# Kernel optimization log

Hardware: AMD Instinct MI355X
Metric: run time of the kernel (lower is better)

Reference implementation:

```python
import jax, jax.numpy as jnp
import numpy as np

N, M = 30000, 32
VX, VY, VZ = 0.2, 0.2, 4.0
XOFF, YOFF, ZOFF = 0.1, -39.9, -1.0  # vx/2+pc_range[0], vy/2+pc_range[1], vz/2+pc_range[2]
EPS = 1e-3
H = 3  # num_heads, head_dim = 3 // 3 = 1


def setup_inputs() -> dict:
    key = jax.random.key(0)
    ks = jax.random.split(key, 13)
    features = jax.random.normal(ks[0], (N, M, 4), jnp.float32)
    num_points = jax.random.randint(ks[1], (N,), 1, M + 1, dtype=jnp.int32)
    coors = jax.random.randint(ks[2], (N, 4), 0, 352, dtype=jnp.int32)
    # PFN layer params (Linear 10->64 no bias, BN1d affine)
    pfn_w = jax.random.normal(ks[3], (10, 64), jnp.float32) * 0.1
    bn_gamma = jnp.ones((64,), jnp.float32)
    bn_beta = jnp.zeros((64,), jnp.float32)
    # PillarAttention: MHA on 3-dim coords, 3 heads of dim 1
    wq = jax.random.normal(ks[4], (3, 3), jnp.float32) * 0.5
    wk = jax.random.normal(ks[5], (3, 3), jnp.float32) * 0.5
    wv = jax.random.normal(ks[6], (3, 3), jnp.float32) * 0.5
    wo = jax.random.normal(ks[7], (3, 3), jnp.float32) * 0.5
    bq = jax.random.normal(ks[8], (3,), jnp.float32) * 0.02
    bk = jax.random.normal(ks[9], (3,), jnp.float32) * 0.02
    bv = jax.random.normal(ks[10], (3,), jnp.float32) * 0.02
    bo = jax.random.normal(ks[11], (3,), jnp.float32) * 0.02
    return dict(features=features, num_points=num_points, coors=coors,
                pfn_w=pfn_w, bn_gamma=bn_gamma, bn_beta=bn_beta,
                wq=wq, wk=wk, wv=wv, wo=wo, bq=bq, bk=bk, bv=bv, bo=bo)


def _pillar_attention(xyz, wq, wk, wv, wo, bq, bk, bv, bo):
    # xyz: (N, M, 3); 3 heads of dim 1 -> per-head score is an outer product
    q = xyz @ wq + bq  # (N, M, 3)
    k = xyz @ wk + bk
    v = xyz @ wv + bv
    # head_dim = 1 => scale = 1/sqrt(1) = 1
    scores = jnp.einsum('nih,njh->nhij', q, k)          # (N, H, M, M)
    attn = jax.nn.softmax(scores, axis=-1)
    out = jnp.einsum('nhij,njh->nih', attn, v)          # (N, M, 3)
    return out @ wo + bo


def reference(features, num_points, coors, pfn_w, bn_gamma, bn_beta,
              wq, wk, wv, wo, bq, bk, bv, bo):
    dtype = features.dtype
    xyz = features[:, :, :3]  # original coords (attn & cluster use these, pre in-place write)

    # PillarAttention on raw xyz, then max over feature dim
    feat_attn = _pillar_attention(xyz, wq, wk, wv, wo, bq, bk, bv, bo)  # (N, M, 3)
    max_attn = jnp.max(feat_attn, axis=-1, keepdims=True)              # (N, M, 1)

    npts = num_points.astype(dtype)[:, None, None]                      # (N,1,1)
    # cluster center offsets (uses original xyz)
    points_mean = jnp.sum(xyz, axis=1, keepdims=True) / npts
    f_cluster = xyz - points_mean                                       # (N, M, 3)

    # voxel center offsets; coors = [batch, z, y, x]
    cf = coors.astype(dtype)
    cx = cf[:, 3] * VX + XOFF
    cy = cf[:, 2] * VY + YOFF
    cz = cf[:, 1] * VZ + ZOFF
    f_center = jnp.stack([xyz[:, :, 0] - cx[:, None],
                          xyz[:, :, 1] - cy[:, None],
                          xyz[:, :, 2] - cz[:, None]], axis=-1)          # (N, M, 3)

    # legacy=True in-place bug: features[:, :, :3] becomes f_center before concat
    feats = jnp.concatenate([f_center, features[:, :, 3:], f_cluster, f_center], axis=-1)  # (N, M, 10)

    # mask out padded points
    mask = (jnp.arange(M)[None, :] < num_points[:, None]).astype(dtype)[:, :, None]
    feats = feats * mask

    # PFNLayer (last_vfe=True): Linear -> BN1d (train-mode stats over N*M) -> LeakyReLU
    x = feats @ pfn_w                                                    # (N, M, 64)
    mean = jnp.mean(x, axis=(0, 1))
    var = jnp.var(x, axis=(0, 1))
    x = (x - mean) * jax.lax.rsqrt(var + EPS) * bn_gamma + bn_beta
    x = jax.nn.leaky_relu(x, negative_slope=0.01)                        # (N, M, 64)

    # attention-weighted max pool fused with plain max pool
    fa = max_attn * x / jnp.sum(max_attn, axis=1, keepdims=True)
    fa = jnp.max(fa, axis=1, keepdims=True)                              # (N, 1, 64)
    fm = jnp.max(x, axis=1, keepdims=True)                               # (N, 1, 64)
    f = (fa + fm) * 0.5
    return f[:, 0, :]                                                    # (N, 64)
```

## Files before the change

kernel.cpp:

```cpp
#include <hip/hip_runtime.h>
#include <float.h>
#include <math.h>

constexpr int NP = 30000;
constexpr int M  = 32;
constexpr float VXc = 0.2f, VYc = 0.2f, VZc = 4.0f;
constexpr float XOFFc = 0.1f, YOFFc = -39.9f, ZOFFc = -1.0f;

typedef __attribute__((ext_vector_type(8)))  short bf16x8;
typedef __attribute__((ext_vector_type(16))) float f32x16;

__device__ __forceinline__ unsigned short f2bf(float x) {
    unsigned int u = __builtin_bit_cast(unsigned int, x);
    u = (u + 0x7fffu + ((u >> 16) & 1u)) >> 16;
    return (unsigned short)u;
}

__global__ __launch_bounds__(256) void stats_kernel(
    const float4* __restrict__ fp,
    const int*    __restrict__ num_points,
    const int*    __restrict__ coors,
    double*       __restrict__ Sout)
{
    float S[35];
#pragma unroll
    for (int k = 0; k < 35; ++k) S[k] = 0.f;

    const int stride = gridDim.x * blockDim.x;
    const int base   = blockIdx.x * blockDim.x + threadIdx.x;

    for (int it = 0; it < 8; ++it) {
        const int p = base + it * stride;
        if (p >= NP * M) continue;
        const int n = p >> 5;
        const int i = p & 31;
        const float4 f = fp[p];

        float sx = f.x, sy = f.y, sz = f.z;
#pragma unroll
        for (int m = 16; m >= 1; m >>= 1) {
            sx += __shfl_xor(sx, m, 32);
            sy += __shfl_xor(sy, m, 32);
            sz += __shfl_xor(sz, m, 32);
        }
        const int npts = num_points[n];
        const float inv = 1.f / (float)npts;
        const int c1 = coors[4 * n + 1], c2 = coors[4 * n + 2], c3 = coors[4 * n + 3];
        const float cx = (float)c3 * VXc + XOFFc;
        const float cy = (float)c2 * VYc + YOFFc;
        const float cz = (float)c1 * VZc + ZOFFc;
        const bool valid = (i < npts);

        float u[7];
        u[0] = valid ? f.x - cx : 0.f;
        u[1] = valid ? f.y - cy : 0.f;
        u[2] = valid ? f.z - cz : 0.f;
        u[3] = valid ? f.w      : 0.f;
        u[4] = valid ? f.x - sx * inv : 0.f;
        u[5] = valid ? f.y - sy * inv : 0.f;
        u[6] = valid ? f.z - sz * inv : 0.f;

#pragma unroll
        for (int k = 0; k < 7; ++k) S[k] += u[k];
        int idx = 7;
#pragma unroll
        for (int k = 0; k < 7; ++k)
#pragma unroll
            for (int l = k; l < 7; ++l)
                S[idx++] += u[k] * u[l];
    }

#pragma unroll
    for (int k = 0; k < 35; ++k) {
#pragma unroll
        for (int m = 32; m >= 1; m >>= 1) S[k] += __shfl_xor(S[k], m, 64);
    }

    __shared__ float part[4][35];
    const int wid = threadIdx.x >> 6, ln = threadIdx.x & 63;
    if (ln == 0) {
#pragma unroll
        for (int k = 0; k < 35; ++k) part[wid][k] = S[k];
    }
    __syncthreads();
    if (threadIdx.x < 35) {
        float t = part[0][threadIdx.x] + part[1][threadIdx.x] +
                  part[2][threadIdx.x] + part[3][threadIdx.x];
        atomicAdd(&Sout[threadIdx.x], (double)t);
    }
}

__global__ __launch_bounds__(128) void affine_kernel(
    const double* __restrict__ S,
    const float*  __restrict__ pfn_w,
    const float*  __restrict__ gamma,
    const float*  __restrict__ beta,
    float*        __restrict__ AB,
    unsigned short* __restrict__ Wpk)
{
    const int tid = threadIdx.x;

    if (tid < 64) {
        const int c = tid;
        double w7[7];
        w7[0] = (double)pfn_w[0 * 64 + c] + (double)pfn_w[7 * 64 + c];
        w7[1] = (double)pfn_w[1 * 64 + c] + (double)pfn_w[8 * 64 + c];
        w7[2] = (double)pfn_w[2 * 64 + c] + (double)pfn_w[9 * 64 + c];
        w7[3] = (double)pfn_w[3 * 64 + c];
        w7[4] = (double)pfn_w[4 * 64 + c];
        w7[5] = (double)pfn_w[5 * 64 + c];
        w7[6] = (double)pfn_w[6 * 64 + c];

        const double invNM = 1.0 / ((double)NP * (double)M);
        double mean = 0.0;
#pragma unroll
        for (int k = 0; k < 7; ++k) mean += S[k] * w7[k];
        mean *= invNM;

        double ex2 = 0.0;
        int idx = 7;
#pragma unroll
        for (int k = 0; k < 7; ++k)
#pragma unroll
            for (int l = k; l < 7; ++l) {
                double t = S[idx++] * w7[k] * w7[l];
                ex2 += (k == l) ? t : 2.0 * t;
            }
        ex2 *= invNM;

        double var = ex2 - mean * mean;
        double a = (double)gamma[c] / sqrt(var + 1e-3);
        AB[c]      = (float)a;
        AB[64 + c] = (float)((double)beta[c] - mean * a);
    }

    {
        const int l = tid & 63;
        const int t = tid >> 6;
        const int half = l >> 5;
        const int n = (l & 31) + 32 * t;
        unsigned short v[8] = {0, 0, 0, 0, 0, 0, 0, 0};
        if (half == 0) {
            float w7[7];
            w7[0] = pfn_w[0 * 64 + n] + pfn_w[7 * 64 + n];
            w7[1] = pfn_w[1 * 64 + n] + pfn_w[8 * 64 + n];
            w7[2] = pfn_w[2 * 64 + n] + pfn_w[9 * 64 + n];
            w7[3] = pfn_w[3 * 64 + n];
            w7[4] = pfn_w[4 * 64 + n];
            w7[5] = pfn_w[5 * 64 + n];
            w7[6] = pfn_w[6 * 64 + n];
#pragma unroll
            for (int j = 0; j < 7; ++j) v[j] = f2bf(w7[j]);
        }
#pragma unroll
        for (int j = 0; j < 8; ++j) Wpk[tid * 8 + j] = v[j];
    }
}

__global__ __launch_bounds__(256) void main_kernel(
    const float4* __restrict__ fp,
    const int*    __restrict__ num_points,
    const int*    __restrict__ coors,
    const float*  __restrict__ AB,
    const unsigned short* __restrict__ Wpk,
    const float*  __restrict__ wq, const float* __restrict__ wk,
    const float*  __restrict__ wv, const float* __restrict__ wo,
    const float*  __restrict__ bq, const float* __restrict__ bk,
    const float*  __restrict__ bv, const float* __restrict__ bo,
    float*        __restrict__ out)
{
    const int tid  = threadIdx.x;
    const int pb   = tid >> 6;
    const int lane = tid & 63;
    const int i    = lane & 31;
    const int half = lane >> 5;
    const int n    = blockIdx.x * 4 + pb;

    __shared__ float2 kv_s[4][3][32];
    __shared__ float  r_s[4][32];

    const float4 f = fp[(size_t)n * M + i];

    float q[3], kk[3], vv[3];
#pragma unroll
    for (int h = 0; h < 3; ++h) {
        q[h]  = f.x * wq[0 * 3 + h] + f.y * wq[1 * 3 + h] + f.z * wq[2 * 3 + h] + bq[h];
        kk[h] = f.x * wk[0 * 3 + h] + f.y * wk[1 * 3 + h] + f.z * wk[2 * 3 + h] + bk[h];
        vv[h] = f.x * wv[0 * 3 + h] + f.y * wv[1 * 3 + h] + f.z * wv[2 * 3 + h] + bv[h];
    }
    if (half == 0) {
#pragma unroll
        for (int h = 0; h < 3; ++h) kv_s[pb][h][i] = make_float2(kk[h], vv[h]);
    }

    float sx = f.x, sy = f.y, sz = f.z;
    float kmx[3], kmn[3];
#pragma unroll
    for (int h = 0; h < 3; ++h) { kmx[h] = kk[h]; kmn[h] = kk[h]; }
#pragma unroll
    for (int m = 16; m >= 1; m >>= 1) {
        sx += __shfl_xor(sx, m, 32);
        sy += __shfl_xor(sy, m, 32);
        sz += __shfl_xor(sz, m, 32);
#pragma unroll
        for (int h = 0; h < 3; ++h) {
            kmx[h] = fmaxf(kmx[h], __shfl_xor(kmx[h], m, 32));
            kmn[h] = fminf(kmn[h], __shfl_xor(kmn[h], m, 32));
        }
    }
    __syncthreads();

    const float LOG2E = 1.4426950408889634f;
    float num[3], den[3];
    const int j0 = half * 16;
#pragma unroll
    for (int h = 0; h < 3; ++h) {
        const float qh2  = q[h] * LOG2E;
        const float mrow = qh2 * (q[h] >= 0.f ? kmx[h] : kmn[h]);
        float d = 0.f, nu = 0.f;
#pragma unroll
        for (int jj = 0; jj < 16; ++jj) {
            float2 kv = kv_s[pb][h][j0 + jj];
            float e = exp2f(__builtin_fmaf(qh2, kv.x, -mrow));
            d  += e;
            nu += e * kv.y;
        }
        num[h] = nu; den[h] = d;
    }
#pragma unroll
    for (int h = 0; h < 3; ++h) {
        num[h] += __shfl_xor(num[h], 32, 64);
        den[h] += __shfl_xor(den[h], 32, 64);
    }
    float o0 = num[0] / den[0], o1 = num[1] / den[1], o2 = num[2] / den[2];

    float fa0 = o0 * wo[0] + o1 * wo[3] + o2 * wo[6] + bo[0];
    float fa1 = o0 * wo[1] + o1 * wo[4] + o2 * wo[7] + bo[1];
    float fa2 = o0 * wo[2] + o1 * wo[5] + o2 * wo[8] + bo[2];
    float ma  = fmaxf(fa0, fmaxf(fa1, fa2));

    float sum_ma = ma;
#pragma unroll
    for (int m = 16; m >= 1; m >>= 1) sum_ma += __shfl_xor(sum_ma, m, 32);
    const float r = ma / sum_ma;
    if (half == 0) r_s[pb][i] = r;

    const int npts = num_points[n];
    const float inv = 1.f / (float)npts;
    const int c1 = coors[4 * n + 1], c2 = coors[4 * n + 2], c3 = coors[4 * n + 3];
    const float cx = (float)c3 * VXc + XOFFc;
    const float cy = (float)c2 * VYc + YOFFc;
    const float cz = (float)c1 * VZc + ZOFFc;
    const bool valid = (i < npts);

    float u[7];
    u[0] = valid ? f.x - cx : 0.f;
    u[1] = valid ? f.y - cy : 0.f;
    u[2] = valid ? f.z - cz : 0.f;
    u[3] = valid ? f.w      : 0.f;
    u[4] = valid ? f.x - sx * inv : 0.f;
    u[5] = valid ? f.y - sy * inv : 0.f;
    u[6] = valid ? f.z - sz * inv : 0.f;

    bf16x8 afr;
#pragma unroll
    for (int e = 0; e < 8; ++e) afr[e] = 0;
    if (half == 0) {
#pragma unroll
        for (int e = 0; e < 7; ++e) afr[e] = (short)f2bf(u[e]);
    }

    const bf16x8 bf0 = *reinterpret_cast<const bf16x8*>(Wpk + (size_t)lane * 8);
    const bf16x8 bf1 = *reinterpret_cast<const bf16x8*>(Wpk + (size_t)(64 + lane) * 8);

    f32x16 acc0, acc1;
#pragma unroll
    for (int e = 0; e < 16; ++e) { acc0[e] = 0.f; acc1[e] = 0.f; }
    acc0 = __builtin_amdgcn_mfma_f32_32x32x16_bf16(afr, bf0, acc0, 0, 0, 0);
    acc1 = __builtin_amdgcn_mfma_f32_32x32x16_bf16(afr, bf1, acc1, 0, 0, 0);

    __syncthreads();

    float rv[16];
#pragma unroll
    for (int rg = 0; rg < 16; ++rg) {
        const int row = (rg & 3) + 8 * (rg >> 2) + 4 * half;
        rv[rg] = r_s[pb][row];
    }

    float res[2];
#pragma unroll
    for (int t = 0; t < 2; ++t) {
        const int c = (lane & 31) + 32 * t;
        const float a = AB[c];
        const float b = AB[64 + c];
        float fm = -FLT_MAX, fav = -FLT_MAX;
#pragma unroll
        for (int rg = 0; rg < 16; ++rg) {
            const float x = (t ? acc1[rg] : acc0[rg]);
            float y = __builtin_fmaf(x, a, b);
            y = fmaxf(y, 0.01f * y);
            fm  = fmaxf(fm, y);
            fav = fmaxf(fav, rv[rg] * y);
        }
        fm  = fmaxf(fm,  __shfl_xor(fm,  32, 64));
        fav = fmaxf(fav, __shfl_xor(fav, 32, 64));
        res[t] = 0.5f * (fav + fm);
    }
    out[(size_t)n * 64 + half * 32 + (lane & 31)] = res[half];
}

extern "C" void kernel_launch(void* const* d_in, const int* in_sizes, int n_in,
                              void* d_out, int out_size, void* d_ws, size_t ws_size,
                              hipStream_t stream) {
    const float4* feats  = (const float4*)d_in[0];
    const int*    npts   = (const int*)d_in[1];
    const int*    coors  = (const int*)d_in[2];
    const float*  pfn_w  = (const float*)d_in[3];
    const float*  gamma  = (const float*)d_in[4];
    const float*  beta   = (const float*)d_in[5];
    const float*  wq     = (const float*)d_in[6];
    const float*  wk     = (const float*)d_in[7];
    const float*  wv     = (const float*)d_in[8];
    const float*  wo     = (const float*)d_in[9];
    const float*  bq     = (const float*)d_in[10];
    const float*  bk     = (const float*)d_in[11];
    const float*  bv     = (const float*)d_in[12];
    const float*  bo     = (const float*)d_in[13];
    float*        out    = (float*)d_out;

    double*         S   = (double*)d_ws;
    float*          AB  = (float*)((char*)d_ws + 384);
    unsigned short* Wpk = (unsigned short*)((char*)d_ws + 896);

    hipMemsetAsync(d_ws, 0, 280, stream);

    stats_kernel<<<480, 256, 0, stream>>>(feats, npts, coors, S);
    affine_kernel<<<1, 128, 0, stream>>>(S, pfn_w, gamma, beta, AB, Wpk);
    main_kernel<<<NP / 4, 256, 0, stream>>>(feats, npts, coors, AB, Wpk,
                                            wq, wk, wv, wo, bq, bk, bv, bo, out);
}
```

Measured before the change: 154.9 us.

## Pack two pillars per wave, drop double atomics and memset for per-block partials

The main kernel now maps each 32-lane half-wave to its own pillar, giving 8 pillars per block. Each lane runs the full 32-key softmax loop over interleaved k/v in shared memory, and four MFMAs use zero-padded A fragments to cover both pillars. The stats kernel writes per-block float partials instead of double atomics, which also removes the memset launch. The affine kernel reduces those partials in double and builds a second Wpk set for the upper-half pillar. Loads are hoisted early and fast rcp/exp2 intrinsics replace division, at the cost of doubled per-lane softmax work and more registers.

```diff
diff --git a/kernel.cpp b/kernel.cpp
--- a/kernel.cpp
+++ b/kernel.cpp
@@ -20,18 +20,15 @@
     const float4* __restrict__ fp,
     const int*    __restrict__ num_points,
     const int*    __restrict__ coors,
-    double*       __restrict__ Sout)
+    float*        __restrict__ Sp)
 {
     float S[35];
 #pragma unroll
     for (int k = 0; k < 35; ++k) S[k] = 0.f;
 
     const int stride = gridDim.x * blockDim.x;
-    const int base   = blockIdx.x * blockDim.x + threadIdx.x;
-
-    for (int it = 0; it < 8; ++it) {
-        const int p = base + it * stride;
-        if (p >= NP * M) continue;
+
+    for (int p = blockIdx.x * blockDim.x + threadIdx.x; p < NP * M; p += stride) {
         const int n = p >> 5;
         const int i = p & 31;
         const float4 f = fp[p];
@@ -44,7 +41,7 @@
             sz += __shfl_xor(sz, m, 32);
         }
         const int npts = num_points[n];
-        const float inv = 1.f / (float)npts;
+        const float inv = __builtin_amdgcn_rcpf((float)npts);
         const int c1 = coors[4 * n + 1], c2 = coors[4 * n + 2], c3 = coors[4 * n + 3];
         const float cx = (float)c3 * VXc + XOFFc;
         const float cy = (float)c2 * VYc + YOFFc;
@@ -84,21 +81,35 @@
     }
     __syncthreads();
     if (threadIdx.x < 35) {
-        float t = part[0][threadIdx.x] + part[1][threadIdx.x] +
-                  part[2][threadIdx.x] + part[3][threadIdx.x];
-        atomicAdd(&Sout[threadIdx.x], (double)t);
+        Sp[blockIdx.x * 35 + threadIdx.x] =
+            part[0][threadIdx.x] + part[1][threadIdx.x] +
+            part[2][threadIdx.x] + part[3][threadIdx.x];
     }
 }
 
 __global__ __launch_bounds__(128) void affine_kernel(
-    const double* __restrict__ S,
-    const float*  __restrict__ pfn_w,
-    const float*  __restrict__ gamma,
-    const float*  __restrict__ beta,
-    float*        __restrict__ AB,
+    const float* __restrict__ Sp,
+    int nsb,
+    const float* __restrict__ pfn_w,
+    const float* __restrict__ gamma,
+    const float* __restrict__ beta,
+    float*       __restrict__ AB,
     unsigned short* __restrict__ Wpk)
 {
+    __shared__ double Sd[35];
     const int tid = threadIdx.x;
+
+    if (tid < 35) {
+        double a0 = 0.0, a1 = 0.0;
+        int b = 0;
+        for (; b + 1 < nsb; b += 2) {
+            a0 += (double)Sp[b * 35 + tid];
+            a1 += (double)Sp[(b + 1) * 35 + tid];
+        }
+        if (b < nsb) a0 += (double)Sp[b * 35 + tid];
+        Sd[tid] = a0 + a1;
+    }
+    __syncthreads();
 
     if (tid < 64) {
         const int c = tid;
@@ -114,7 +125,7 @@
         const double invNM = 1.0 / ((double)NP * (double)M);
         double mean = 0.0;
 #pragma unroll
-        for (int k = 0; k < 7; ++k) mean += S[k] * w7[k];
+        for (int k = 0; k < 7; ++k) mean += Sd[k] * w7[k];
         mean *= invNM;
 
         double ex2 = 0.0;
@@ -123,7 +134,7 @@
         for (int k = 0; k < 7; ++k)
 #pragma unroll
             for (int l = k; l < 7; ++l) {
-                double t = S[idx++] * w7[k] * w7[l];
+                double t = Sd[idx++] * w7[k] * w7[l];
                 ex2 += (k == l) ? t : 2.0 * t;
             }
         ex2 *= invNM;
@@ -134,13 +145,16 @@
         AB[64 + c] = (float)((double)beta[c] - mean * a);
     }
 
-    {
-        const int l = tid & 63;
-        const int t = tid >> 6;
+#pragma unroll
+    for (int it = 0; it < 2; ++it) {
+        const int s = it * 128 + tid;
+        const int v = s >> 7;
+        const int t = (s >> 6) & 1;
+        const int l = s & 63;
         const int half = l >> 5;
         const int n = (l & 31) + 32 * t;
-        unsigned short v[8] = {0, 0, 0, 0, 0, 0, 0, 0};
-        if (half == 0) {
+        unsigned short val[8] = {0, 0, 0, 0, 0, 0, 0, 0};
+        if (half == v) {
             float w7[7];
             w7[0] = pfn_w[0 * 64 + n] + pfn_w[7 * 64 + n];
             w7[1] = pfn_w[1 * 64 + n] + pfn_w[8 * 64 + n];
@@ -150,10 +164,10 @@
             w7[5] = pfn_w[5 * 64 + n];
             w7[6] = pfn_w[6 * 64 + n];
 #pragma unroll
-            for (int j = 0; j < 7; ++j) v[j] = f2bf(w7[j]);
-        }
-#pragma unroll
-        for (int j = 0; j < 8; ++j) Wpk[tid * 8 + j] = v[j];
+            for (int j = 0; j < 7; ++j) val[j] = f2bf(w7[j]);
+        }
+#pragma unroll
+        for (int j = 0; j < 8; ++j) Wpk[s * 8 + j] = val[j];
     }
 }
 
@@ -170,16 +184,25 @@
     float*        __restrict__ out)
 {
     const int tid  = threadIdx.x;
-    const int pb   = tid >> 6;
+    const int wave = tid >> 6;
     const int lane = tid & 63;
+    const int half = lane >> 5;
     const int i    = lane & 31;
-    const int half = lane >> 5;
-    const int n    = blockIdx.x * 4 + pb;
-
-    __shared__ float2 kv_s[4][3][32];
-    __shared__ float  r_s[4][32];
+    const int p    = wave * 2 + half;
+    const int n    = blockIdx.x * 8 + p;
+
+    __shared__ float kv_s[8][32][8];
+    __shared__ float r_s[8][32];
 
     const float4 f = fp[(size_t)n * M + i];
+    const int npts = num_points[n];
+    const int c1 = coors[4 * n + 1], c2 = coors[4 * n + 2], c3 = coors[4 * n + 3];
+    const float a_t0 = AB[i], a_t1 = AB[32 + i];
+    const float b_t0 = AB[64 + i], b_t1 = AB[96 + i];
+    const bf16x8 bfA0 = *reinterpret_cast<const bf16x8*>(Wpk + (size_t)(  0 + lane) * 8);
+    const bf16x8 bfA1 = *reinterpret_cast<const bf16x8*>(Wpk + (size_t)( 64 + lane) * 8);
+    const bf16x8 bfB0 = *reinterpret_cast<const bf16x8*>(Wpk + (size_t)(128 + lane) * 8);
+    const bf16x8 bfB1 = *reinterpret_cast<const bf16x8*>(Wpk + (size_t)(192 + lane) * 8);
 
     float q[3], kk[3], vv[3];
 #pragma unroll
@@ -188,10 +211,8 @@
         kk[h] = f.x * wk[0 * 3 + h] + f.y * wk[1 * 3 + h] + f.z * wk[2 * 3 + h] + bk[h];
         vv[h] = f.x * wv[0 * 3 + h] + f.y * wv[1 * 3 + h] + f.z * wv[2 * 3 + h] + bv[h];
     }
-    if (half == 0) {
-#pragma unroll
-        for (int h = 0; h < 3; ++h) kv_s[pb][h][i] = make_float2(kk[h], vv[h]);
-    }
+    *reinterpret_cast<float4*>(&kv_s[p][i][0]) = make_float4(kk[0], vv[0], kk[1], vv[1]);
+    *reinterpret_cast<float2*>(&kv_s[p][i][4]) = make_float2(kk[2], vv[2]);
 
     float sx = f.x, sy = f.y, sz = f.z;
     float kmx[3], kmn[3];
@@ -211,28 +232,27 @@
     __syncthreads();
 
     const float LOG2E = 1.4426950408889634f;
-    float num[3], den[3];
-    const int j0 = half * 16;
+    float qh2[3], mrow[3];
 #pragma unroll
     for (int h = 0; h < 3; ++h) {
-        const float qh2  = q[h] * LOG2E;
-        const float mrow = qh2 * (q[h] >= 0.f ? kmx[h] : kmn[h]);
-        float d = 0.f, nu = 0.f;
-#pragma unroll
-        for (int jj = 0; jj < 16; ++jj) {
-            float2 kv = kv_s[pb][h][j0 + jj];
-            float e = exp2f(__builtin_fmaf(qh2, kv.x, -mrow));
-            d  += e;
-            nu += e * kv.y;
-        }
-        num[h] = nu; den[h] = d;
-    }
-#pragma unroll
-    for (int h = 0; h < 3; ++h) {
-        num[h] += __shfl_xor(num[h], 32, 64);
-        den[h] += __shfl_xor(den[h], 32, 64);
-    }
-    float o0 = num[0] / den[0], o1 = num[1] / den[1], o2 = num[2] / den[2];
+        qh2[h]  = q[h] * LOG2E;
+        mrow[h] = qh2[h] * (q[h] >= 0.f ? kmx[h] : kmn[h]);
+    }
+    float den[3] = {0.f, 0.f, 0.f}, num[3] = {0.f, 0.f, 0.f};
+#pragma unroll
+    for (int j = 0; j < 32; ++j) {
+        const float4 kv01 = *reinterpret_cast<const float4*>(&kv_s[p][j][0]);
+        const float2 kv2  = *reinterpret_cast<const float2*>(&kv_s[p][j][4]);
+        float e0 = __builtin_amdgcn_exp2f(__builtin_fmaf(qh2[0], kv01.x, -mrow[0]));
+        float e1 = __builtin_amdgcn_exp2f(__builtin_fmaf(qh2[1], kv01.z, -mrow[1]));
+        float e2 = __builtin_amdgcn_exp2f(__builtin_fmaf(qh2[2], kv2.x,  -mrow[2]));
+        den[0] += e0; num[0] = __builtin_fmaf(e0, kv01.y, num[0]);
+        den[1] += e1; num[1] = __builtin_fmaf(e1, kv01.w, num[1]);
+        den[2] += e2; num[2] = __builtin_fmaf(e2, kv2.y,  num[2]);
+    }
+    const float o0 = num[0] * __builtin_amdgcn_rcpf(den[0]);
+    const float o1 = num[1] * __builtin_amdgcn_rcpf(den[1]);
+    const float o2 = num[2] * __builtin_amdgcn_rcpf(den[2]);
 
     float fa0 = o0 * wo[0] + o1 * wo[3] + o2 * wo[6] + bo[0];
     float fa1 = o0 * wo[1] + o1 * wo[4] + o2 * wo[7] + bo[1];
@@ -242,12 +262,9 @@
     float sum_ma = ma;
 #pragma unroll
     for (int m = 16; m >= 1; m >>= 1) sum_ma += __shfl_xor(sum_ma, m, 32);
-    const float r = ma / sum_ma;
-    if (half == 0) r_s[pb][i] = r;
-
-    const int npts = num_points[n];
-    const float inv = 1.f / (float)npts;
-    const int c1 = coors[4 * n + 1], c2 = coors[4 * n + 2], c3 = coors[4 * n + 3];
+    r_s[p][i] = ma * __builtin_amdgcn_rcpf(sum_ma);
+
+    const float inv = __builtin_amdgcn_rcpf((float)npts);
     const float cx = (float)c3 * VXc + XOFFc;
     const float cy = (float)c2 * VYc + YOFFc;
     const float cz = (float)c1 * VZc + ZOFFc;
@@ -262,52 +279,83 @@
     u[5] = valid ? f.y - sy * inv : 0.f;
     u[6] = valid ? f.z - sz * inv : 0.f;
 
-    bf16x8 afr;
-#pragma unroll
-    for (int e = 0; e < 8; ++e) afr[e] = 0;
-    if (half == 0) {
-#pragma unroll
-        for (int e = 0; e < 7; ++e) afr[e] = (short)f2bf(u[e]);
-    }
-
-    const bf16x8 bf0 = *reinterpret_cast<const bf16x8*>(Wpk + (size_t)lane * 8);
-    const bf16x8 bf1 = *reinterpret_cast<const bf16x8*>(Wpk + (size_t)(64 + lane) * 8);
-
-    f32x16 acc0, acc1;
-#pragma unroll
-    for (int e = 0; e < 16; ++e) { acc0[e] = 0.f; acc1[e] = 0.f; }
-    acc0 = __builtin_amdgcn_mfma_f32_32x32x16_bf16(afr, bf0, acc0, 0, 0, 0);
-    acc1 = __builtin_amdgcn_mfma_f32_32x32x16_bf16(afr, bf1, acc1, 0, 0, 0);
+    unsigned int w32[4];
+    w32[0] = (unsigned int)f2bf(u[0]) | ((unsigned int)f2bf(u[1]) << 16);
+    w32[1] = (unsigned int)f2bf(u[2]) | ((unsigned int)f2bf(u[3]) << 16);
+    w32[2] = (unsigned int)f2bf(u[4]) | ((unsigned int)f2bf(u[5]) << 16);
+    w32[3] = (unsigned int)f2bf(u[6]);
+
+    union { unsigned int w[4]; bf16x8 v; } ua, ub;
+#pragma unroll
+    for (int e = 0; e < 4; ++e) {
+        ua.w[e] = (half == 0) ? w32[e] : 0u;
+        ub.w[e] = (half == 1) ? w32[e] : 0u;
+    }
+
+    f32x16 accA0, accA1, accB0, accB1;
+#pragma unroll
+    for (int e = 0; e < 16; ++e) { accA0[e] = 0.f; accA1[e] = 0.f; accB0[e] = 0.f; accB1[e] = 0.f; }
+    accA0 = __builtin_amdgcn_mfma_f32_32x32x16_bf16(ua.v, bfA0, accA0, 0, 0, 0);
+    accA1 = __builtin_amdgcn_mfma_f32_32x32x16_bf16(ua.v, bfA1, accA1, 0, 0, 0);
+    accB0 = __builtin_amdgcn_mfma_f32_32x32x16_bf16(ub.v, bfB0, accB0, 0, 0, 0);
+    accB1 = __builtin_amdgcn_mfma_f32_32x32x16_bf16(ub.v, bfB1, accB1, 0, 0, 0);
 
     __syncthreads();
 
-    float rv[16];
-#pragma unroll
-    for (int rg = 0; rg < 16; ++rg) {
-        const int row = (rg & 3) + 8 * (rg >> 2) + 4 * half;
-        rv[rg] = r_s[pb][row];
-    }
-
-    float res[2];
-#pragma unroll
-    for (int t = 0; t < 2; ++t) {
-        const int c = (lane & 31) + 32 * t;
-        const float a = AB[c];
-        const float b = AB[64 + c];
-        float fm = -FLT_MAX, fav = -FLT_MAX;
+    const int pA = wave * 2;
+    const int nA = blockIdx.x * 8 + pA;
+
+    {
+        float4 rg4[4];
+#pragma unroll
+        for (int g = 0; g < 4; ++g)
+            rg4[g] = *reinterpret_cast<const float4*>(&r_s[pA][g * 8 + 4 * half]);
+
+        float fm0 = -FLT_MAX, fv0 = -FLT_MAX, fm1 = -FLT_MAX, fv1 = -FLT_MAX;
 #pragma unroll
         for (int rg = 0; rg < 16; ++rg) {
-            const float x = (t ? acc1[rg] : acc0[rg]);
-            float y = __builtin_fmaf(x, a, b);
-            y = fmaxf(y, 0.01f * y);
-            fm  = fmaxf(fm, y);
-            fav = fmaxf(fav, rv[rg] * y);
-        }
-        fm  = fmaxf(fm,  __shfl_xor(fm,  32, 64));
-        fav = fmaxf(fav, __shfl_xor(fav, 32, 64));
-        res[t] = 0.5f * (fav + fm);
-    }
-    out[(size_t)n * 64 + half * 32 + (lane & 31)] = res[half];
+            const float rr = rg4[rg >> 2][rg & 3];
+            float y0 = __builtin_fmaf(accA0[rg], a_t0, b_t0);
+            y0 = fmaxf(y0, 0.01f * y0);
+            fm0 = fmaxf(fm0, y0); fv0 = fmaxf(fv0, rr * y0);
+            float y1 = __builtin_fmaf(accA1[rg], a_t1, b_t1);
+            y1 = fmaxf(y1, 0.01f * y1);
+            fm1 = fmaxf(fm1, y1); fv1 = fmaxf(fv1, rr * y1);
+        }
+        fm0 = fmaxf(fm0, __shfl_xor(fm0, 32, 64));
+        fv0 = fmaxf(fv0, __shfl_xor(fv0, 32, 64));
+        fm1 = fmaxf(fm1, __shfl_xor(fm1, 32, 64));
+        fv1 = fmaxf(fv1, __shfl_xor(fv1, 32, 64));
+        const float res = (half == 0) ? 0.5f * (fv0 + fm0) : 0.5f * (fv1 + fm1);
+        out[(size_t)nA * 64 + 32 * half + i] = res;
+    }
+
+    {
+        const int pB = pA + 1;
+        const int nB = nA + 1;
+        float4 rg4[4];
+#pragma unroll
+        for (int g = 0; g < 4; ++g)
+            rg4[g] = *reinterpret_cast<const float4*>(&r_s[pB][g * 8 + 4 * half]);
+
+        float fm0 = -FLT_MAX, fv0 = -FLT_MAX, fm1 = -FLT_MAX, fv1 = -FLT_MAX;
+#pragma unroll
+        for (int rg = 0; rg < 16; ++rg) {
+            const float rr = rg4[rg >> 2][rg & 3];
+            float y0 = __builtin_fmaf(accB0[rg], a_t0, b_t0);
+            y0 = fmaxf(y0, 0.01f * y0);
+            fm0 = fmaxf(fm0, y0); fv0 = fmaxf(fv0, rr * y0);
+            float y1 = __builtin_fmaf(accB1[rg], a_t1, b_t1);
+            y1 = fmaxf(y1, 0.01f * y1);
+            fm1 = fmaxf(fm1, y1); fv1 = fmaxf(fv1, rr * y1);
+        }
+        fm0 = fmaxf(fm0, __shfl_xor(fm0, 32, 64));
+        fv0 = fmaxf(fv0, __shfl_xor(fv0, 32, 64));
+        fm1 = fmaxf(fm1, __shfl_xor(fm1, 32, 64));
+        fv1 = fmaxf(fv1, __shfl_xor(fv1, 32, 64));
+        const float res = (half == 0) ? 0.5f * (fv0 + fm0) : 0.5f * (fv1 + fm1);
+        out[(size_t)nB * 64 + 32 * half + i] = res;
+    }
 }
 
 extern "C" void kernel_launch(void* const* d_in, const int* in_sizes, int n_in,
@@ -329,14 +377,19 @@
     const float*  bo     = (const float*)d_in[13];
     float*        out    = (float*)d_out;
 
-    double*         S   = (double*)d_ws;
-    float*          AB  = (float*)((char*)d_ws + 384);
-    unsigned short* Wpk = (unsigned short*)((char*)d_ws + 896);
-
-    hipMemsetAsync(d_ws, 0, 280, stream);
-
-    stats_kernel<<<480, 256, 0, stream>>>(feats, npts, coors, S);
-    affine_kernel<<<1, 128, 0, stream>>>(S, pfn_w, gamma, beta, AB, Wpk);
-    main_kernel<<<NP / 4, 256, 0, stream>>>(feats, npts, coors, AB, Wpk,
+    int nsb = 480;
+    if (ws_size > 0 && ws_size < (size_t)(480 * 140 + 8192)) {
+        size_t avail = ws_size > 8192 ? ws_size - 8192 : 140;
+        int fit = (int)(avail / 140);
+        nsb = fit < 1 ? 1 : (fit > 480 ? 480 : fit);
+    }
+    size_t ab_off  = ((size_t)(nsb * 140) + 255) & ~(size_t)255;
+    float*          Sp  = (float*)d_ws;
+    float*          AB  = (float*)((char*)d_ws + ab_off);
+    unsigned short* Wpk = (unsigned short*)((char*)d_ws + ab_off + 512);
+
+    stats_kernel<<<nsb, 256, 0, stream>>>(feats, npts, coors, Sp);
+    affine_kernel<<<1, 128, 0, stream>>>(Sp, nsb, pfn_w, gamma, beta, AB, Wpk);
+    main_kernel<<<NP / 8, 256, 0, stream>>>(feats, npts, coors, AB, Wpk,
                                             wq, wk, wv, wo, bq, bk, bv, bo, out);
 }
```

Result: slower. 199.1 us (+28.6%).
